# Kernel tuning notes

Measured on AMD Instinct MI355X. Metric: run time of the kernel, lower is better.

The kernel has to match this reference:

```python
import jax, jax.numpy as jnp
import numpy as np

D = 768
EPS = 1e-5

def _layernorm(x, g, b):
    mu = jnp.mean(x, axis=-1, keepdims=True)
    var = jnp.mean(jnp.square(x - mu), axis=-1, keepdims=True)
    return (x - mu) * jax.lax.rsqrt(var + EPS) * g + b

def setup_inputs() -> dict:
    key = jax.random.key(0)
    ks = jax.random.split(key, 12)
    s = 1.0 / np.sqrt(D)
    x = jax.random.normal(ks[0], (8, 2048, D), dtype=jnp.float32)
    Wq = jax.random.uniform(ks[1], (D, D), jnp.float32, -s, s)
    bq = jax.random.uniform(ks[2], (D,), jnp.float32, -s, s)
    Wk = jax.random.uniform(ks[3], (D, D), jnp.float32, -s, s)
    bk = jax.random.uniform(ks[4], (D,), jnp.float32, -s, s)
    Wv = jax.random.uniform(ks[5], (D, D), jnp.float32, -s, s)
    bv = jax.random.uniform(ks[6], (D,), jnp.float32, -s, s)
    W1 = jax.random.uniform(ks[7], (D, D), jnp.float32, -s, s)
    b1 = jax.random.uniform(ks[8], (D,), jnp.float32, -s, s)
    W2 = jax.random.uniform(ks[9], (D, D), jnp.float32, -s, s)
    b2 = jax.random.uniform(ks[10], (D,), jnp.float32, -s, s)
    g_n1 = jnp.ones((D,), jnp.float32); be_n1 = jnp.zeros((D,), jnp.float32)
    g_n2 = jnp.ones((D,), jnp.float32); be_n2 = jnp.zeros((D,), jnp.float32)
    return {"x": x, "Wq": Wq, "bq": bq, "Wk": Wk, "bk": bk, "Wv": Wv, "bv": bv,
            "W1": W1, "b1": b1, "W2": W2, "b2": b2,
            "g_n1": g_n1, "be_n1": be_n1, "g_n2": g_n2, "be_n2": be_n2}

def reference(x, Wq, bq, Wk, bk, Wv, bv, W1, b1, W2, b2, g_n1, be_n1, g_n2, be_n2):
    # pre-norm single-head self-attention (scores materialized as in source)
    h = _layernorm(x, g_n1, be_n1)
    q = h @ Wq.T + bq  # [B,S,D]
    k = h @ Wk.T + bk
    v = h @ Wv.T + bv
    scores = jnp.einsum('bsd,btd->bst', q, k) / jnp.sqrt(jnp.float32(D))
    attn = jax.nn.softmax(scores, axis=-1)
    x = jnp.einsum('bst,btd->bsd', attn, v) + x
    # MLP: two Linear(d,d) each followed by exact GELU (matches source MLP)
    h = _layernorm(x, g_n2, be_n2)
    h = jax.nn.gelu(h @ W1.T + b1, approximate=False)
    h = jax.nn.gelu(h @ W2.T + b2, approximate=False)
    return h + x
```

## Files before the change

kernel.cpp:

```cpp
#include <hip/hip_runtime.h>
#include <cstdint>
#include <cstddef>

#define D_MODEL 768
#define NBATCH 8
#define SEQLEN 2048
#define NROWS (NBATCH*SEQLEN)

typedef __attribute__((ext_vector_type(4))) float  f32x4;
typedef __attribute__((ext_vector_type(8))) __bf16 bf16x8;
typedef __attribute__((ext_vector_type(4))) __bf16 bf16x4;

#define MFMA16(a,b,c) __builtin_amdgcn_mfma_f32_16x16x32_bf16(a,b,c,0,0,0)
#define SCALE 0.03608439182435161f
#define AS1 __attribute__((address_space(1)))
#define AS3 __attribute__((address_space(3)))

static constexpr size_t SZ_ACT = (size_t)NROWS * D_MODEL * 2;
static constexpr size_t OFF_Q    = 0;
static constexpr size_t OFF_K    = OFF_Q + SZ_ACT;
static constexpr size_t OFF_VT   = OFF_K + SZ_ACT;
static constexpr size_t OFF_X2   = OFF_VT + SZ_ACT;
static constexpr size_t OFF_W    = OFF_X2 + SZ_ACT;
static constexpr size_t OFF_POOL = OFF_W + (size_t)5*589824*2;

__device__ __forceinline__ float gelu_exact(float x) {
  return 0.5f * x * (1.0f + erff(x * 0.70710678118654752f));
}

__device__ __forceinline__ int xcd_remap(int p, int chunk) {
  return (p & 7) * chunk + (p >> 3);
}

__global__ __launch_bounds__(256) void k_cvt5(
    const float* __restrict__ s0, const float* __restrict__ s1,
    const float* __restrict__ s2, const float* __restrict__ s3,
    const float* __restrict__ s4, __bf16* __restrict__ dst)
{
  const int wsel = blockIdx.y;
  const float* s = wsel==0 ? s0 : wsel==1 ? s1 : wsel==2 ? s2 : wsel==3 ? s3 : s4;
  const size_t i = ((size_t)blockIdx.x*256 + threadIdx.x)*4;
  float4 v = *(const float4*)(s + i);
  bf16x4 o;
  o[0] = (__bf16)v.x; o[1] = (__bf16)v.y; o[2] = (__bf16)v.z; o[3] = (__bf16)v.w;
  *(bf16x4*)(dst + (size_t)wsel*589824 + i) = o;
}

__global__ __launch_bounds__(256) void k_layernorm(
    const float* __restrict__ x, const float* __restrict__ g,
    const float* __restrict__ be, __bf16* __restrict__ out)
{
  const int row  = blockIdx.x*4 + (threadIdx.x>>6);
  const int lane = threadIdx.x & 63;
  const float4* xr = (const float4*)(x + (size_t)row*D_MODEL);
  float4 v[3];
  float s = 0.f, ss = 0.f;
#pragma unroll
  for (int j=0;j<3;j++){
    v[j] = xr[lane + 64*j];
    s  += v[j].x + v[j].y + v[j].z + v[j].w;
    ss += v[j].x*v[j].x + v[j].y*v[j].y + v[j].z*v[j].z + v[j].w*v[j].w;
  }
#pragma unroll
  for (int d=1; d<64; d<<=1){ s += __shfl_xor(s,d); ss += __shfl_xor(ss,d); }
  const float mu   = s  * (1.f/768.f);
  const float var  = ss * (1.f/768.f) - mu*mu;
  const float rstd = rsqrtf(var + 1e-5f);
  __bf16* orow = out + (size_t)row*D_MODEL;
#pragma unroll
  for (int j=0;j<3;j++){
    const int c0 = (lane + 64*j)*4;
    bf16x4 o;
    o[0] = (__bf16)((v[j].x - mu)*rstd*g[c0+0] + be[c0+0]);
    o[1] = (__bf16)((v[j].y - mu)*rstd*g[c0+1] + be[c0+1]);
    o[2] = (__bf16)((v[j].z - mu)*rstd*g[c0+2] + be[c0+2]);
    o[3] = (__bf16)((v[j].w - mu)*rstd*g[c0+3] + be[c0+3]);
    *(bf16x4*)(orow + c0) = o;
  }
}

__global__ __launch_bounds__(256) void k_layernorm_b(
    const __bf16* __restrict__ x, const float* __restrict__ g,
    const float* __restrict__ be, __bf16* __restrict__ out)
{
  const int row  = blockIdx.x*4 + (threadIdx.x>>6);
  const int lane = threadIdx.x & 63;
  const __bf16* xr = x + (size_t)row*D_MODEL;
  float f[12];
  float s = 0.f, ss = 0.f;
#pragma unroll
  for (int j=0;j<3;j++){
    bf16x4 v = *(const bf16x4*)(xr + (lane + 64*j)*4);
#pragma unroll
    for (int e=0;e<4;e++){
      const float fv = (float)v[e];
      f[j*4+e] = fv; s += fv; ss += fv*fv;
    }
  }
#pragma unroll
  for (int d=1; d<64; d<<=1){ s += __shfl_xor(s,d); ss += __shfl_xor(ss,d); }
  const float mu   = s  * (1.f/768.f);
  const float var  = ss * (1.f/768.f) - mu*mu;
  const float rstd = rsqrtf(var + 1e-5f);
  __bf16* orow = out + (size_t)row*D_MODEL;
#pragma unroll
  for (int j=0;j<3;j++){
    const int c0 = (lane + 64*j)*4;
    bf16x4 o;
#pragma unroll
    for (int e=0;e<4;e++) o[e] = (__bf16)((f[j*4+e] - mu)*rstd*g[c0+e] + be[c0+e]);
    *(bf16x4*)(orow + c0) = o;
  }
}

__global__ __launch_bounds__(256) void k_rowsum(
    const __bf16* __restrict__ P, float* __restrict__ inv)
{
  const int row  = blockIdx.x*4 + (threadIdx.x>>6);
  const int lane = threadIdx.x & 63;
  const __bf16* pr = P + (size_t)row*SEQLEN + lane*32;
  float s = 0.f;
#pragma unroll
  for (int j=0;j<4;j++){
    bf16x8 v = *(const bf16x8*)(pr + j*8);
#pragma unroll
    for (int e=0;e<8;e++) s += (float)v[e];
  }
#pragma unroll
  for (int d=1; d<64; d<<=1) s += __shfl_xor(s, d);
  if (lane==0) inv[row] = 1.0f / s;
}

template<int NT>
__device__ __forceinline__ void gemm_core_rp(
    __bf16* __restrict__ As, __bf16* __restrict__ Bs,
    const __bf16* __restrict__ Asrc, const int ldA,
    const __bf16* __restrict__ Bsrc, const int ldB,
    f32x4 (&acc)[4][4])
{
  const int tid = threadIdx.x, w = tid>>6, lane = tid&63;
  const int wr = w>>1, wc = w&1, l16 = lane&15, l4 = lane>>4;

  const int rql   = l16>>1;
  const int rslot = (((l16&1)<<2) + l4) ^ rql;
  const int roff  = rql*64 + rslot*8;

  const int su  = (lane&7) ^ (lane>>3);
  const int ss_ = (su>>2)&1;
  const int sg_ = su&3;
  const int srw = 2*(lane>>3) + ss_;
  const int sco = sg_*8;

#pragma unroll
  for (int mi=0;mi<4;mi++)
#pragma unroll
    for (int ni=0;ni<4;ni++)
      acc[mi][ni] = (f32x4){0.f,0.f,0.f,0.f};

#define STGRP(T_) { \
    const int kb_ = (T_)*32; \
    const int sb_ = ((T_)&1)*4096; \
    _Pragma("unroll") \
    for (int i_=0;i_<2;i_++){ \
      const int ii_ = w + i_*4; \
      const int rg_ = ii_*16 + srw; \
      __builtin_amdgcn_global_load_lds((const AS1 void*)(Asrc + (size_t)rg_*ldA + kb_ + sco), (AS3 void*)(As + sb_ + ii_*512), 16, 0, 0); \
      __builtin_amdgcn_global_load_lds((const AS1 void*)(Bsrc + (size_t)rg_*ldB + kb_ + sco), (AS3 void*)(Bs + sb_ + ii_*512), 16, 0, 0); \
    } }

  STGRP(0) STGRP(1)

  for (int t=0; t<NT; ++t){
    if (t+1 < NT) asm volatile("s_waitcnt vmcnt(4)" ::: "memory");
    else          asm volatile("s_waitcnt vmcnt(0)" ::: "memory");
    __builtin_amdgcn_s_barrier();
    const int sb = (t&1)*4096;
    bf16x8 af[4], bq[4];
#pragma unroll
    for (int mi=0;mi<4;mi++)
      af[mi] = *(const bf16x8*)(As + sb + (wr*32 + mi*8)*64 + roff);
#pragma unroll
    for (int ni=0;ni<4;ni++)
      bq[ni] = *(const bf16x8*)(Bs + sb + (wc*32 + ni*8)*64 + roff);
    asm volatile("s_waitcnt lgkmcnt(0)" ::: "memory");
    __builtin_amdgcn_sched_barrier(0);
    __builtin_amdgcn_s_barrier();
    if (t+2 < NT) STGRP(t+2)
    __builtin_amdgcn_s_setprio(1);
#pragma unroll
    for (int mi=0;mi<4;mi++)
#pragma unroll
      for (int ni=0;ni<4;ni++)
        acc[mi][ni] = MFMA16(af[mi], bq[ni], acc[mi][ni]);
    __builtin_amdgcn_s_setprio(0);
  }
#undef STGRP
}

__global__ __launch_bounds__(256) void k_qkv(
    const __bf16* __restrict__ A, const __bf16* __restrict__ W,
    const float* __restrict__ bq, const float* __restrict__ bk, const float* __restrict__ bv,
    __bf16* __restrict__ Cq, __bf16* __restrict__ Ck, __bf16* __restrict__ vT)
{
  __shared__ __bf16 As[2*4096];
  __shared__ __bf16 Bs[2*4096];
  const int L = xcd_remap(blockIdx.x, 288);
  const int bm = L/18, bn = L%18;
  f32x4 acc[4][4];
  gemm_core_rp<24>(As, Bs, A + (size_t)bm*128*D_MODEL, D_MODEL, W + (size_t)bn*128*D_MODEL, D_MODEL, acc);
  const int tid = threadIdx.x, w=tid>>6, lane=tid&63;
  const int wr=w>>1, wc=w&1, l16=lane&15, l4=lane>>4;
  const int seg = bn/6;
  const int colb = (bn%6)*128 + wc*64;
  const int row0 = bm*128 + wr*64;
  if (seg < 2){
    const float* bias = seg==0 ? bq : bk;
    __bf16* C = seg==0 ? Cq : Ck;
#pragma unroll
    for (int ni=0;ni<4;ni++){
      const int col = colb + ni*16 + l16;
      const float bb = bias[col];
#pragma unroll
      for (int mi=0;mi<4;mi++)
#pragma unroll
        for (int r=0;r<4;r++){
          const int row = row0 + mi*16 + l4*4 + r;
          float v = acc[mi][ni][r] + bb;
          if (seg==0) v *= SCALE;
          C[(size_t)row*D_MODEL + col] = (__bf16)v;
        }
    }
  } else {
    const int b = row0 >> 11;
    const int trow0 = row0 & 2047;
    __bf16* vtb = vT + (size_t)b*D_MODEL*SEQLEN;
#pragma unroll
    for (int ni=0;ni<4;ni++){
      const int col = colb + ni*16 + l16;
      const float bb = bv[col];
#pragma unroll
      for (int mi=0;mi<4;mi++){
        bf16x4 o;
#pragma unroll
        for (int r=0;r<4;r++) o[r] = (__bf16)(acc[mi][ni][r] + bb);
        *(bf16x4*)(vtb + (size_t)col*SEQLEN + trow0 + mi*16 + l4*4) = o;
      }
    }
  }
}

__global__ __launch_bounds__(256) void k_s(
    const __bf16* __restrict__ Q, const __bf16* __restrict__ K,
    __bf16* __restrict__ S, int chunk)
{
  __shared__ __bf16 As[2*4096];
  __shared__ __bf16 Bs[2*4096];
  const int L = xcd_remap(blockIdx.x, chunk);
  const int batch = L>>8, r = L&255;
  const int bm = r>>4, bn = r&15;
  const size_t bo = (size_t)batch * SEQLEN * D_MODEL;
  f32x4 acc[4][4];
  gemm_core_rp<24>(As, Bs, Q + bo + (size_t)bm*128*D_MODEL, D_MODEL, K + bo + (size_t)bn*128*D_MODEL, D_MODEL, acc);
  const int tid = threadIdx.x, w=tid>>6, lane=tid&63;
  const int wr=w>>1, wc=w&1, l16=lane&15, l4=lane>>4;
  __bf16* Sb = S + (size_t)batch*SEQLEN*SEQLEN;
  const int row0 = bm*128 + wr*64, col0 = bn*128 + wc*64;
#pragma unroll
  for (int ni=0;ni<4;ni++){
    const int col = col0 + ni*16 + l16;
#pragma unroll
    for (int mi=0;mi<4;mi++)
#pragma unroll
      for (int r2=0;r2<4;r2++)
        Sb[(size_t)(row0 + mi*16 + l4*4 + r2)*SEQLEN + col] = (__bf16)__expf(acc[mi][ni][r2]);
  }
}

__global__ __launch_bounds__(256) void k_pv(
    const __bf16* __restrict__ P, const float* __restrict__ inv,
    const __bf16* __restrict__ VT,
    const float* __restrict__ x, __bf16* __restrict__ x2, int bbase, int chunk)
{
  __shared__ __bf16 As[2*4096];
  __shared__ __bf16 Bs[2*4096];
  const int L = xcd_remap(blockIdx.x, chunk);
  const int by = L/96, r = L%96;
  const int bm = r/6, bn = r%6;
  const int bidx = bbase + by;
  f32x4 acc[4][4];
  gemm_core_rp<64>(As, Bs, P + (size_t)by*SEQLEN*SEQLEN + (size_t)bm*128*SEQLEN, SEQLEN,
                   VT + (size_t)bidx*D_MODEL*SEQLEN + (size_t)bn*128*SEQLEN, SEQLEN, acc);
  const int tid = threadIdx.x, w=tid>>6, lane=tid&63;
  const int wr=w>>1, wc=w&1, l16=lane&15, l4=lane>>4;
  __syncthreads();
  float* rs = (float*)Bs;
  if (tid < 128) rs[tid] = inv[(size_t)by*SEQLEN + bm*128 + tid];
  __syncthreads();
  const size_t row0 = (size_t)bidx*SEQLEN + bm*128 + wr*64;
  const int col0 = bn*128 + wc*64;
#pragma unroll
  for (int ni=0;ni<4;ni++){
    const int col = col0 + ni*16 + l16;
#pragma unroll
    for (int mi=0;mi<4;mi++)
#pragma unroll
      for (int r2=0;r2<4;r2++){
        const size_t row = row0 + mi*16 + l4*4 + r2;
        const float iv = rs[wr*64 + mi*16 + l4*4 + r2];
        x2[row*D_MODEL + col] = (__bf16)(acc[mi][ni][r2]*iv + x[row*D_MODEL + col]);
      }
  }
}

template<int RES>
__global__ __launch_bounds__(256) void k_mlp(
    const __bf16* __restrict__ A, const __bf16* __restrict__ W,
    const float* __restrict__ bias, const __bf16* __restrict__ resid, void* __restrict__ out)
{
  __shared__ __bf16 As[2*4096];
  __shared__ __bf16 Bs[2*4096];
  const int L = xcd_remap(blockIdx.x, 96);
  const int bm = L/6, bn = L%6;
  f32x4 acc[4][4];
  gemm_core_rp<24>(As, Bs, A + (size_t)bm*128*D_MODEL, D_MODEL, W + (size_t)bn*128*D_MODEL, D_MODEL, acc);
  const int tid = threadIdx.x, w=tid>>6, lane=tid&63;
  const int wr=w>>1, wc=w&1, l16=lane&15, l4=lane>>4;
  const int row0 = bm*128 + wr*64, col0 = bn*128 + wc*64;
#pragma unroll
  for (int ni=0;ni<4;ni++){
    const int col = col0 + ni*16 + l16;
    const float bb = bias[col];
#pragma unroll
    for (int mi=0;mi<4;mi++)
#pragma unroll
      for (int r=0;r<4;r++){
        const int row = row0 + mi*16 + l4*4 + r;
        float v = gelu_exact(acc[mi][ni][r] + bb);
        if (RES) ((float*)out)[(size_t)row*D_MODEL + col] = v + (float)resid[(size_t)row*D_MODEL + col];
        else     ((__bf16*)out)[(size_t)row*D_MODEL + col] = (__bf16)v;
      }
  }
}

extern "C" void kernel_launch(void* const* d_in, const int* in_sizes, int n_in,
                              void* d_out, int out_size, void* d_ws, size_t ws_size,
                              hipStream_t stream)
{
  const float* x   = (const float*)d_in[0];
  const float* Wq  = (const float*)d_in[1];
  const float* bq  = (const float*)d_in[2];
  const float* Wk  = (const float*)d_in[3];
  const float* bk  = (const float*)d_in[4];
  const float* Wv  = (const float*)d_in[5];
  const float* bv  = (const float*)d_in[6];
  const float* W1  = (const float*)d_in[7];
  const float* b1  = (const float*)d_in[8];
  const float* W2  = (const float*)d_in[9];
  const float* b2  = (const float*)d_in[10];
  const float* g1  = (const float*)d_in[11];
  const float* be1 = (const float*)d_in[12];
  const float* g2  = (const float*)d_in[13];
  const float* be2 = (const float*)d_in[14];
  (void)in_sizes; (void)n_in; (void)out_size;

  char* ws = (char*)d_ws;
  __bf16*   qb  = (__bf16*)(ws + OFF_Q);
  __bf16*   kb  = (__bf16*)(ws + OFF_K);
  __bf16*   vT  = (__bf16*)(ws + OFF_VT);
  __bf16*   x2  = (__bf16*)(ws + OFF_X2);
  __bf16*   wbf = (__bf16*)(ws + OFF_W);
  __bf16*   h1  = (__bf16*)(ws + OFF_POOL);
  __bf16*   Sp  = (__bf16*)(ws + OFF_POOL);
  __bf16*   h2  = h1;
  __bf16*   h3  = qb;

  const size_t szS8 = (size_t)NBATCH*SEQLEN*SEQLEN*2;
  const size_t szI8 = (size_t)NROWS*4;
  const bool big = ws_size >= OFF_POOL + szS8 + szI8;

  k_cvt5<<<dim3(576,5,1),256,0,stream>>>(Wq,Wk,Wv,W1,W2,wbf);
  k_layernorm<<<dim3(4096),256,0,stream>>>(x, g1, be1, h1);
  k_qkv<<<dim3(2304),256,0,stream>>>(h1, wbf, bq, bk, bv, qb, kb, vT);

  if (big){
    float* inv = (float*)(ws + OFF_POOL + szS8);
    k_s<<<dim3(2048),256,0,stream>>>(qb, kb, Sp, 256);
    k_rowsum<<<dim3(4096),256,0,stream>>>(Sp, inv);
    k_pv<<<dim3(768),256,0,stream>>>(Sp, inv, vT, x, x2, 0, 96);
  } else {
    float* inv = (float*)(ws + OFF_POOL + (size_t)4*SEQLEN*SEQLEN*2);
    for (int c=0;c<2;c++){
      const size_t qoff = (size_t)c*4*SEQLEN*D_MODEL;
      k_s<<<dim3(1024),256,0,stream>>>(qb + qoff, kb + qoff, Sp, 128);
      k_rowsum<<<dim3(2048),256,0,stream>>>(Sp, inv);
      k_pv<<<dim3(384),256,0,stream>>>(Sp, inv, vT, x, x2, c*4, 48);
    }
  }

  k_layernorm_b<<<dim3(4096),256,0,stream>>>(x2, g2, be2, h2);
  k_mlp<0><<<dim3(768),256,0,stream>>>(h2, wbf + (size_t)3*589824, b1, nullptr, h3);
  k_mlp<1><<<dim3(768),256,0,stream>>>(h3, wbf + (size_t)4*589824, b2, x2, d_out);
}
```

Baseline: 359.6 us.

## Switch GEMMs to 256x256 tiles with 8 waves and phased prefetch

Replaces the 128x128, 4-wave GEMM core with a 256x256, 8-wave core that uses K=64 steps. Each K step is split into four phases, and each phase issues part of the next tile's global-to-LDS loads, interleaved with MFMA sub-blocks. The larger tiles raise arithmetic intensity and cut redundant operand loads. The cost is much smaller grids: 192 blocks for the PV and MLP kernels, fewer than the CU count. Each block also holds 128KB of LDS at one block per CU, which risks leaving CUs idle and exposing load latency.

After: 434.0 us. +20.7%, slower.

```diff
diff --git a/kernel.cpp b/kernel.cpp
--- a/kernel.cpp
+++ b/kernel.cpp
@@ -131,88 +131,95 @@
   if (lane==0) inv[row] = 1.0f / s;
 }
 
+#define STG(DST, SRC, LD, T_, Q_) \
+  __builtin_amdgcn_global_load_lds( \
+    (const AS1 void*)((SRC) + (size_t)((Q_)*64 + w*8 + sro)*(LD) + (T_)*64 + sgr), \
+    (AS3 void*)((DST) + (((T_)&1)*16384) + ((Q_)*64 + w*8)*64), 16, 0, 0);
+
 template<int NT>
-__device__ __forceinline__ void gemm_core_rp(
+__device__ __forceinline__ void gemm8(
     __bf16* __restrict__ As, __bf16* __restrict__ Bs,
     const __bf16* __restrict__ Asrc, const int ldA,
     const __bf16* __restrict__ Bsrc, const int ldB,
-    f32x4 (&acc)[4][4])
+    f32x4 (&acc)[8][4])
 {
   const int tid = threadIdx.x, w = tid>>6, lane = tid&63;
-  const int wr = w>>1, wc = w&1, l16 = lane&15, l4 = lane>>4;
-
-  const int rql   = l16>>1;
-  const int rslot = (((l16&1)<<2) + l4) ^ rql;
-  const int roff  = rql*64 + rslot*8;
-
-  const int su  = (lane&7) ^ (lane>>3);
-  const int ss_ = (su>>2)&1;
-  const int sg_ = su&3;
-  const int srw = 2*(lane>>3) + ss_;
-  const int sco = sg_*8;
-
-#pragma unroll
-  for (int mi=0;mi<4;mi++)
+  const int wr = w>>2, wc = w&3, l16 = lane&15, l4 = lane>>4;
+  const int sro = lane>>3;
+  const int sgr = ((lane&7) ^ (lane>>3))*8;
+  const int rx  = l16 & 7;
+
+#pragma unroll
+  for (int mi=0;mi<8;mi++)
 #pragma unroll
     for (int ni=0;ni<4;ni++)
       acc[mi][ni] = (f32x4){0.f,0.f,0.f,0.f};
 
-#define STGRP(T_) { \
-    const int kb_ = (T_)*32; \
-    const int sb_ = ((T_)&1)*4096; \
-    _Pragma("unroll") \
-    for (int i_=0;i_<2;i_++){ \
-      const int ii_ = w + i_*4; \
-      const int rg_ = ii_*16 + srw; \
-      __builtin_amdgcn_global_load_lds((const AS1 void*)(Asrc + (size_t)rg_*ldA + kb_ + sco), (AS3 void*)(As + sb_ + ii_*512), 16, 0, 0); \
-      __builtin_amdgcn_global_load_lds((const AS1 void*)(Bsrc + (size_t)rg_*ldB + kb_ + sco), (AS3 void*)(Bs + sb_ + ii_*512), 16, 0, 0); \
-    } }
-
-  STGRP(0) STGRP(1)
+  STG(As, Asrc, ldA, 0, 0) STG(As, Asrc, ldA, 0, 2)
+  STG(Bs, Bsrc, ldB, 0, 0) STG(Bs, Bsrc, ldB, 0, 1)
+  STG(Bs, Bsrc, ldB, 0, 2) STG(Bs, Bsrc, ldB, 0, 3)
+  STG(As, Asrc, ldA, 0, 1) STG(As, Asrc, ldA, 0, 3)
 
   for (int t=0; t<NT; ++t){
-    if (t+1 < NT) asm volatile("s_waitcnt vmcnt(4)" ::: "memory");
-    else          asm volatile("s_waitcnt vmcnt(0)" ::: "memory");
-    __builtin_amdgcn_s_barrier();
-    const int sb = (t&1)*4096;
-    bf16x8 af[4], bq[4];
-#pragma unroll
-    for (int mi=0;mi<4;mi++)
-      af[mi] = *(const bf16x8*)(As + sb + (wr*32 + mi*8)*64 + roff);
-#pragma unroll
-    for (int ni=0;ni<4;ni++)
-      bq[ni] = *(const bf16x8*)(Bs + sb + (wc*32 + ni*8)*64 + roff);
-    asm volatile("s_waitcnt lgkmcnt(0)" ::: "memory");
-    __builtin_amdgcn_sched_barrier(0);
-    __builtin_amdgcn_s_barrier();
-    if (t+2 < NT) STGRP(t+2)
-    __builtin_amdgcn_s_setprio(1);
-#pragma unroll
-    for (int mi=0;mi<4;mi++)
-#pragma unroll
-      for (int ni=0;ni<4;ni++)
-        acc[mi][ni] = MFMA16(af[mi], bq[ni], acc[mi][ni]);
-    __builtin_amdgcn_s_setprio(0);
-  }
-#undef STGRP
-}
-
-__global__ __launch_bounds__(256) void k_qkv(
+    const int pb = (t&1)*16384;
+    const bool pf = (t+1 < NT);
+#pragma unroll
+    for (int p=0;p<4;p++){
+      if (p==0) asm volatile("s_waitcnt vmcnt(2)" ::: "memory");
+      if (p==2){
+        if (pf) asm volatile("s_waitcnt vmcnt(4)" ::: "memory");
+        else    asm volatile("s_waitcnt vmcnt(0)" ::: "memory");
+      }
+      __builtin_amdgcn_s_barrier();
+      const int qm = p>>1, qn = p&1;
+      bf16x8 af[4][2], bfr[2][2];
+#pragma unroll
+      for (int mi=0;mi<4;mi++)
+#pragma unroll
+        for (int kk=0;kk<2;kk++)
+          af[mi][kk] = *(const bf16x8*)(As + pb + (wr*128 + (qm*4+mi)*16 + l16)*64 + ((kk*4+l4)^rx)*8);
+#pragma unroll
+      for (int ni=0;ni<2;ni++)
+#pragma unroll
+        for (int kk=0;kk<2;kk++)
+          bfr[ni][kk] = *(const bf16x8*)(Bs + pb + (wc*64 + (qn*2+ni)*16 + l16)*64 + ((kk*4+l4)^rx)*8);
+      if (pf){
+        if (p==0){ STG(As, Asrc, ldA, t+1, 0) STG(As, Asrc, ldA, t+1, 2) }
+        if (p==1){ STG(Bs, Bsrc, ldB, t+1, 0) STG(Bs, Bsrc, ldB, t+1, 1) }
+        if (p==2){ STG(Bs, Bsrc, ldB, t+1, 2) STG(Bs, Bsrc, ldB, t+1, 3) }
+        if (p==3){ STG(As, Asrc, ldA, t+1, 1) STG(As, Asrc, ldA, t+1, 3) }
+      }
+      asm volatile("s_waitcnt lgkmcnt(0)" ::: "memory");
+      __builtin_amdgcn_sched_barrier(0);
+      __builtin_amdgcn_s_setprio(1);
+#pragma unroll
+      for (int kk=0;kk<2;kk++)
+#pragma unroll
+        for (int mi=0;mi<4;mi++)
+#pragma unroll
+          for (int ni=0;ni<2;ni++)
+            acc[qm*4+mi][qn*2+ni] = MFMA16(af[mi][kk], bfr[ni][kk], acc[qm*4+mi][qn*2+ni]);
+      __builtin_amdgcn_s_setprio(0);
+    }
+  }
+}
+
+__global__ __launch_bounds__(512,1) void k_qkv(
     const __bf16* __restrict__ A, const __bf16* __restrict__ W,
     const float* __restrict__ bq, const float* __restrict__ bk, const float* __restrict__ bv,
     __bf16* __restrict__ Cq, __bf16* __restrict__ Ck, __bf16* __restrict__ vT)
 {
-  __shared__ __bf16 As[2*4096];
-  __shared__ __bf16 Bs[2*4096];
-  const int L = xcd_remap(blockIdx.x, 288);
-  const int bm = L/18, bn = L%18;
-  f32x4 acc[4][4];
-  gemm_core_rp<24>(As, Bs, A + (size_t)bm*128*D_MODEL, D_MODEL, W + (size_t)bn*128*D_MODEL, D_MODEL, acc);
+  __shared__ __bf16 As[2*16384];
+  __shared__ __bf16 Bs[2*16384];
+  const int L = xcd_remap(blockIdx.x, 72);
+  const int bm = L/9, bn = L%9;
+  f32x4 acc[8][4];
+  gemm8<12>(As, Bs, A + (size_t)bm*256*D_MODEL, D_MODEL, W + (size_t)bn*256*D_MODEL, D_MODEL, acc);
   const int tid = threadIdx.x, w=tid>>6, lane=tid&63;
-  const int wr=w>>1, wc=w&1, l16=lane&15, l4=lane>>4;
-  const int seg = bn/6;
-  const int colb = (bn%6)*128 + wc*64;
-  const int row0 = bm*128 + wr*64;
+  const int wr=w>>2, wc=w&3, l16=lane&15, l4=lane>>4;
+  const int seg = bn/3;
+  const int colb = (bn%3)*256 + wc*64;
+  const int row0 = bm*256 + wr*128;
   if (seg < 2){
     const float* bias = seg==0 ? bq : bk;
     __bf16* C = seg==0 ? Cq : Ck;
@@ -221,7 +228,7 @@
       const int col = colb + ni*16 + l16;
       const float bb = bias[col];
 #pragma unroll
-      for (int mi=0;mi<4;mi++)
+      for (int mi=0;mi<8;mi++)
 #pragma unroll
         for (int r=0;r<4;r++){
           const int row = row0 + mi*16 + l4*4 + r;
@@ -231,15 +238,15 @@
         }
     }
   } else {
-    const int b = row0 >> 11;
-    const int trow0 = row0 & 2047;
+    const int b = bm >> 3;
+    const int trow0 = (bm & 7)*256 + wr*128;
     __bf16* vtb = vT + (size_t)b*D_MODEL*SEQLEN;
 #pragma unroll
     for (int ni=0;ni<4;ni++){
       const int col = colb + ni*16 + l16;
       const float bb = bv[col];
 #pragma unroll
-      for (int mi=0;mi<4;mi++){
+      for (int mi=0;mi<8;mi++){
         bf16x4 o;
 #pragma unroll
         for (int r=0;r<4;r++) o[r] = (__bf16)(acc[mi][ni][r] + bb);
@@ -249,89 +256,90 @@
   }
 }
 
-__global__ __launch_bounds__(256) void k_s(
+__global__ __launch_bounds__(512,1) void k_s(
     const __bf16* __restrict__ Q, const __bf16* __restrict__ K,
     __bf16* __restrict__ S, int chunk)
 {
-  __shared__ __bf16 As[2*4096];
-  __shared__ __bf16 Bs[2*4096];
+  __shared__ __bf16 As[2*16384];
+  __shared__ __bf16 Bs[2*16384];
   const int L = xcd_remap(blockIdx.x, chunk);
-  const int batch = L>>8, r = L&255;
-  const int bm = r>>4, bn = r&15;
+  const int batch = L>>6, r = L&63;
+  const int bm = r>>3, bn = r&7;
   const size_t bo = (size_t)batch * SEQLEN * D_MODEL;
-  f32x4 acc[4][4];
-  gemm_core_rp<24>(As, Bs, Q + bo + (size_t)bm*128*D_MODEL, D_MODEL, K + bo + (size_t)bn*128*D_MODEL, D_MODEL, acc);
+  f32x4 acc[8][4];
+  gemm8<12>(As, Bs, Q + bo + (size_t)bm*256*D_MODEL, D_MODEL, K + bo + (size_t)bn*256*D_MODEL, D_MODEL, acc);
   const int tid = threadIdx.x, w=tid>>6, lane=tid&63;
-  const int wr=w>>1, wc=w&1, l16=lane&15, l4=lane>>4;
+  const int wr=w>>2, wc=w&3, l16=lane&15, l4=lane>>4;
   __bf16* Sb = S + (size_t)batch*SEQLEN*SEQLEN;
-  const int row0 = bm*128 + wr*64, col0 = bn*128 + wc*64;
+  const int row0 = bm*256 + wr*128, col0 = bn*256 + wc*64;
 #pragma unroll
   for (int ni=0;ni<4;ni++){
     const int col = col0 + ni*16 + l16;
 #pragma unroll
-    for (int mi=0;mi<4;mi++)
+    for (int mi=0;mi<8;mi++)
 #pragma unroll
       for (int r2=0;r2<4;r2++)
         Sb[(size_t)(row0 + mi*16 + l4*4 + r2)*SEQLEN + col] = (__bf16)__expf(acc[mi][ni][r2]);
   }
 }
 
-__global__ __launch_bounds__(256) void k_pv(
+__global__ __launch_bounds__(512,1) void k_pv(
     const __bf16* __restrict__ P, const float* __restrict__ inv,
     const __bf16* __restrict__ VT,
     const float* __restrict__ x, __bf16* __restrict__ x2, int bbase, int chunk)
 {
-  __shared__ __bf16 As[2*4096];
-  __shared__ __bf16 Bs[2*4096];
+  __shared__ __bf16 As[2*16384];
+  __shared__ __bf16 Bs[2*16384];
   const int L = xcd_remap(blockIdx.x, chunk);
-  const int by = L/96, r = L%96;
-  const int bm = r/6, bn = r%6;
+  const int by = L/24, r = L%24;
+  const int bm = r/3, bn = r%3;
   const int bidx = bbase + by;
-  f32x4 acc[4][4];
-  gemm_core_rp<64>(As, Bs, P + (size_t)by*SEQLEN*SEQLEN + (size_t)bm*128*SEQLEN, SEQLEN,
-                   VT + (size_t)bidx*D_MODEL*SEQLEN + (size_t)bn*128*SEQLEN, SEQLEN, acc);
+  f32x4 acc[8][4];
+  gemm8<32>(As, Bs, P + (size_t)by*SEQLEN*SEQLEN + (size_t)bm*256*SEQLEN, SEQLEN,
+            VT + (size_t)bidx*D_MODEL*SEQLEN + (size_t)bn*256*SEQLEN, SEQLEN, acc);
   const int tid = threadIdx.x, w=tid>>6, lane=tid&63;
-  const int wr=w>>1, wc=w&1, l16=lane&15, l4=lane>>4;
+  const int wr=w>>2, wc=w&3, l16=lane&15, l4=lane>>4;
   __syncthreads();
-  float* rs = (float*)Bs;
-  if (tid < 128) rs[tid] = inv[(size_t)by*SEQLEN + bm*128 + tid];
+  float* rs = (float*)As;
+  if (tid < 256) rs[tid] = inv[(size_t)by*SEQLEN + bm*256 + tid];
   __syncthreads();
-  const size_t row0 = (size_t)bidx*SEQLEN + bm*128 + wr*64;
-  const int col0 = bn*128 + wc*64;
+  const size_t row0 = (size_t)bidx*SEQLEN + bm*256 + wr*128;
+  const int rloc0 = wr*128;
+  const int col0 = bn*256 + wc*64;
 #pragma unroll
   for (int ni=0;ni<4;ni++){
     const int col = col0 + ni*16 + l16;
 #pragma unroll
-    for (int mi=0;mi<4;mi++)
+    for (int mi=0;mi<8;mi++)
 #pragma unroll
       for (int r2=0;r2<4;r2++){
         const size_t row = row0 + mi*16 + l4*4 + r2;
-        const float iv = rs[wr*64 + mi*16 + l4*4 + r2];
+        const float iv = rs[rloc0 + mi*16 + l4*4 + r2];
         x2[row*D_MODEL + col] = (__bf16)(acc[mi][ni][r2]*iv + x[row*D_MODEL + col]);
       }
   }
 }
 
 template<int RES>
-__global__ __launch_bounds__(256) void k_mlp(
+__global__ __launch_bounds__(512,1) void k_mlp(
     const __bf16* __restrict__ A, const __bf16* __restrict__ W,
     const float* __restrict__ bias, const __bf16* __restrict__ resid, void* __restrict__ out)
 {
-  __shared__ __bf16 As[2*4096];
-  __shared__ __bf16 Bs[2*4096];
-  const int L = xcd_remap(blockIdx.x, 96);
-  const int bm = L/6, bn = L%6;
-  f32x4 acc[4][4];
-  gemm_core_rp<24>(As, Bs, A + (size_t)bm*128*D_MODEL, D_MODEL, W + (size_t)bn*128*D_MODEL, D_MODEL, acc);
+  __shared__ __bf16 As[2*16384];
+  __shared__ __bf16 Bs[2*16384];
+  const int L = xcd_remap(blockIdx.x, 24);
+  const int bm = L/3, bn = L%3;
+  f32x4 acc[8][4];
+  gemm8<12>(As, Bs, A + (size_t)bm*256*D_MODEL, D_MODEL, W + (size_t)bn*256*D_MODEL, D_MODEL, acc);
   const int tid = threadIdx.x, w=tid>>6, lane=tid&63;
-  const int wr=w>>1, wc=w&1, l16=lane&15, l4=lane>>4;
-  const int row0 = bm*128 + wr*64, col0 = bn*128 + wc*64;
+  const int wr=w>>2, wc=w&3, l16=lane&15, l4=lane>>4;
+  const int row0 = bm*256 + wr*128, col0 = bn*256 + wc*64;
 #pragma unroll
   for (int ni=0;ni<4;ni++){
     const int col = col0 + ni*16 + l16;
     const float bb = bias[col];
 #pragma unroll
-    for (int mi=0;mi<4;mi++)
+    for (int mi=0;mi<8;mi++)
 #pragma unroll
       for (int r=0;r<4;r++){
         const int row = row0 + mi*16 + l4*4 + r;
@@ -380,24 +388,24 @@
 
   k_cvt5<<<dim3(576,5,1),256,0,stream>>>(Wq,Wk,Wv,W1,W2,wbf);
   k_layernorm<<<dim3(4096),256,0,stream>>>(x, g1, be1, h1);
-  k_qkv<<<dim3(2304),256,0,stream>>>(h1, wbf, bq, bk, bv, qb, kb, vT);
+  k_qkv<<<dim3(576),512,0,stream>>>(h1, wbf, bq, bk, bv, qb, kb, vT);
 
   if (big){
     float* inv = (float*)(ws + OFF_POOL + szS8);
-    k_s<<<dim3(2048),256,0,stream>>>(qb, kb, Sp, 256);
+    k_s<<<dim3(512),512,0,stream>>>(qb, kb, Sp, 64);
     k_rowsum<<<dim3(4096),256,0,stream>>>(Sp, inv);
-    k_pv<<<dim3(768),256,0,stream>>>(Sp, inv, vT, x, x2, 0, 96);
+    k_pv<<<dim3(192),512,0,stream>>>(Sp, inv, vT, x, x2, 0, 24);
   } else {
     float* inv = (float*)(ws + OFF_POOL + (size_t)4*SEQLEN*SEQLEN*2);
     for (int c=0;c<2;c++){
       const size_t qoff = (size_t)c*4*SEQLEN*D_MODEL;
-      k_s<<<dim3(1024),256,0,stream>>>(qb + qoff, kb + qoff, Sp, 128);
+      k_s<<<dim3(256),512,0,stream>>>(qb + qoff, kb + qoff, Sp, 32);
       k_rowsum<<<dim3(2048),256,0,stream>>>(Sp, inv);
-      k_pv<<<dim3(384),256,0,stream>>>(Sp, inv, vT, x, x2, c*4, 48);
+      k_pv<<<dim3(96),512,0,stream>>>(Sp, inv, vT, x, x2, c*4, 12);
     }
   }
 
   k_layernorm_b<<<dim3(4096),256,0,stream>>>(x2, g2, be2, h2);
-  k_mlp<0><<<dim3(768),256,0,stream>>>(h2, wbf + (size_t)3*589824, b1, nullptr, h3);
-  k_mlp<1><<<dim3(768),256,0,stream>>>(h3, wbf + (size_t)4*589824, b2, x2, d_out);
-}
+  k_mlp<0><<<dim3(192),512,0,stream>>>(h2, wbf + (size_t)3*589824, b1, nullptr, h3);
+  k_mlp<1><<<dim3(192),512,0,stream>>>(h3, wbf + (size_t)4*589824, b2, x2, d_out);
+}
```
